# Kernel optimization log

Measured on AMD Instinct MI355X. Metric: run time of the kernel, lower is better.

Reference implementation:

```python
import jax, jax.numpy as jnp
import numpy as np

KINEMATIC_CHAIN = [[0, 2, 5, 8, 11], [0, 1, 4, 7, 10], [0, 3, 6, 9, 12, 15],
                   [9, 14, 17, 19, 21], [9, 13, 16, 18, 20]]
PATHS = [c[1:] for c in KINEMATIC_CHAIN]  # nb_joints == 22 branch


def _gauss_integral(s1, e1, s2, e2):
    # s1,e1,s2,e2: (..., 3) broadcastable; returns (...,) GLI per segment pair
    r13 = s2 - s1
    r14 = e2 - s1
    r23 = s2 - e1
    r24 = e2 - e1
    r12 = e1 - s1
    r34 = e2 - s2
    faces = jnp.stack([jnp.cross(r13, r14), jnp.cross(r14, r24),
                       jnp.cross(r24, r23), jnp.cross(r23, r13)], axis=-2)  # (...,4,3)
    norms = jnp.linalg.norm(faces, axis=-1, keepdims=True)
    nf = jnp.where(norms > 0, faces / jnp.maximum(norms, 1e-30), 0.0)
    dots = jnp.sum(nf * jnp.roll(nf, -1, axis=-2), axis=-1)  # (...,4)
    dots = jnp.clip(dots, -1.0 + 1e-7, 1.0 - 1e-7)
    gli = jnp.sum(jnp.arcsin(dots), axis=-1)
    sign = jnp.sum(jnp.cross(r34, r12) * r13, axis=-1)
    gli = gli * jnp.where(sign <= 0, -1.0, 1.0)
    return gli / (4.0 * jnp.pi)


def _gli_motion(motion1, motion2):
    # motion: (B, F, J, 3) -> (B, F, P*P) summed GLI per path pair
    pair_sums = []
    for p1 in PATHS:
        p1 = np.asarray(p1)
        s1 = motion1[:, :, p1[:-1], None, :]   # (B,F,n1,1,3)
        e1 = motion1[:, :, p1[1:], None, :]
        for p2 in PATHS:
            p2 = np.asarray(p2)
            s2 = motion2[:, :, None, p2[:-1], :]  # (B,F,1,n2,3)
            e2 = motion2[:, :, None, p2[1:], :]
            g = _gauss_integral(s1, e1, s2, e2)   # (B,F,n1,n2)
            pair_sums.append(jnp.sum(g, axis=(-1, -2)))
    return jnp.stack(pair_sums, axis=-1)  # (B, F, 25)


def setup_inputs() -> dict:
    key = jax.random.key(0)
    k1, k2 = jax.random.split(key)
    B, F, J = 32, 1024, 22
    return {
        "motion1": jax.random.normal(k1, (B, F, J, 3), dtype=jnp.float32),
        "motion2": jax.random.normal(k2, (B, F, J, 3), dtype=jnp.float32),
    }


def reference(motion1, motion2):
    gli = _gli_motion(motion1, motion2)            # (B, F, 25)
    vel = jnp.abs(gli[:, 1:] - gli[:, :-1])        # (B, F-1, 25)
    return jnp.max(vel, axis=-1)                   # (B, F-1)
```

## Files before the change

### kernel.cpp

```cpp
#include <hip/hip_runtime.h>
#include <hip/hip_bf16.h>


#define NF 1024
#define NB 32
#define FPB 16

__constant__ int c_seg_a[16] = {2,5,8,  1,4,7,  3,6,9,12,  14,17,19,  13,16,18};
__constant__ int c_seg_b[16] = {5,8,11, 4,7,10, 6,9,12,15, 17,19,21,  16,18,20};
__constant__ int c_seg_p[16] = {0,0,0,  1,1,1,  2,2,2,2,   3,3,3,     4,4,4};
__constant__ int c_grp_s[5]  = {0, 3, 6, 10, 13};
__constant__ int c_grp_e[5]  = {3, 6, 10, 13, 16};

struct V3 { float x, y, z; };

__device__ __forceinline__ V3 vsub(V3 a, V3 b) { return {a.x-b.x, a.y-b.y, a.z-b.z}; }
__device__ __forceinline__ V3 vcross(V3 a, V3 b) {
    return {fmaf(a.y, b.z, -a.z*b.y), fmaf(a.z, b.x, -a.x*b.z), fmaf(a.x, b.y, -a.y*b.x)};
}
__device__ __forceinline__ float vdot(V3 a, V3 b) {
    return fmaf(a.x, b.x, fmaf(a.y, b.y, a.z*b.z));
}

__device__ __forceinline__ float fast_asin(float x) {
    float ax = fabsf(x);
    float p = fmaf(ax, -0.0012624911f, 0.0066700901f);
    p = fmaf(ax, p, -0.0170881256f);
    p = fmaf(ax, p,  0.0308918810f);
    p = fmaf(ax, p, -0.0501743046f);
    p = fmaf(ax, p,  0.0889789874f);
    p = fmaf(ax, p, -0.2145988016f);
    p = fmaf(ax, p,  1.5707963050f);
    float r = fmaf(-__builtin_amdgcn_sqrtf(1.0f - ax), p, 1.57079632679f);
    return copysignf(r, x);
}

__global__ __launch_bounds__(256)
void gli_kernel(const float* __restrict__ m1, const float* __restrict__ m2,
                float* __restrict__ gli)
{
    __shared__ float smem[FPB * 66 * 2];
    float* j1 = smem;
    float* j2 = smem + FPB * 66;

    const int f0 = blockIdx.x * FPB;
    const int b  = blockIdx.y;
    const int t  = threadIdx.x;

    const size_t mbase = ((size_t)b * NF + f0) * 66;
    for (int i = t; i < FPB * 66; i += 256) {
        j1[i] = m1[mbase + i];
        j2[i] = m2[mbase + i];
    }
    __syncthreads();

    const int k  = t >> 4;
    const int i1 = t & 15;
    const float* J1 = j1 + k * 66;
    const float* J2 = j2 + k * 66;

    const int a1 = c_seg_a[i1] * 3, b1 = c_seg_b[i1] * 3;
    V3 S1{J1[a1], J1[a1+1], J1[a1+2]};
    V3 E1{J1[b1], J1[b1+1], J1[b1+2]};
    V3 r12 = vsub(E1, S1);

    float acc[5] = {0.0f, 0.0f, 0.0f, 0.0f, 0.0f};

#pragma unroll
    for (int i2 = 0; i2 < 16; ++i2) {
        const int a2 = c_seg_a[i2] * 3, b2 = c_seg_b[i2] * 3;
        V3 S2{J2[a2], J2[a2+1], J2[a2+2]};
        V3 E2{J2[b2], J2[b2+1], J2[b2+2]};

        V3 r13 = vsub(S2, S1);
        V3 r14 = vsub(E2, S1);
        V3 r23 = vsub(S2, E1);
        V3 r24 = vsub(E2, E1);
        V3 r34 = vsub(E2, S2);

        V3 c0 = vcross(r13, r14);
        V3 c1 = vcross(r14, r24);
        V3 c2 = vcross(r24, r23);
        V3 c3 = vcross(r23, r13);

        float n0 = vdot(c0, c0), n1 = vdot(c1, c1);
        float n2 = vdot(c2, c2), n3 = vdot(c3, c3);

        float q01 = n0 * n1, q12 = n1 * n2, q23 = n2 * n3, q30 = n3 * n0;
        float i01 = (q01 > 0.0f) ? __builtin_amdgcn_rsqf(q01) : 0.0f;
        float i12 = (q12 > 0.0f) ? __builtin_amdgcn_rsqf(q12) : 0.0f;
        float i23 = (q23 > 0.0f) ? __builtin_amdgcn_rsqf(q23) : 0.0f;
        float i30 = (q30 > 0.0f) ? __builtin_amdgcn_rsqf(q30) : 0.0f;

        const float lo = -1.0f + 1e-7f, hi = 1.0f - 1e-7f;
        float d0 = fminf(fmaxf(vdot(c0, c1) * i01, lo), hi);
        float d1 = fminf(fmaxf(vdot(c1, c2) * i12, lo), hi);
        float d2 = fminf(fmaxf(vdot(c2, c3) * i23, lo), hi);
        float d3 = fminf(fmaxf(vdot(c3, c0) * i30, lo), hi);

        float g = fast_asin(d0) + fast_asin(d1) + fast_asin(d2) + fast_asin(d3);

        float sgn = vdot(vcross(r34, r12), r13);
        g = (sgn <= 0.0f) ? -g : g;

        acc[c_seg_p[i2]] += g;
    }

    __syncthreads();

    float* red = smem;
#pragma unroll
    for (int p = 0; p < 5; ++p)
        red[(k * 16 + i1) * 5 + p] = acc[p] * 0.07957747154594767f;
    __syncthreads();

    for (int item = t; item < FPB * 25; item += 256) {
        int kk  = item / 25;
        int bin = item - kk * 25;
        int p1 = bin / 5, p2 = bin - p1 * 5;
        float s = 0.0f;
        for (int i = c_grp_s[p1]; i < c_grp_e[p1]; ++i)
            s += red[(kk * 16 + i) * 5 + p2];
        gli[((size_t)b * NF + f0 + kk) * 25 + bin] = s;
    }
}

__global__ __launch_bounds__(256)
void vel_kernel(const float* __restrict__ gli, float* __restrict__ out)
{
    const int f = blockIdx.x * blockDim.x + threadIdx.x;
    const int b = blockIdx.y;
    if (f >= NF - 1) return;

    const float* p0 = gli + ((size_t)b * NF + f) * 25;
    float m = 0.0f;
#pragma unroll
    for (int p = 0; p < 25; ++p)
        m = fmaxf(m, fabsf(p0[p + 25] - p0[p]));
    out[(size_t)b * (NF - 1) + f] = m;
}

extern "C" void kernel_launch(void* const* d_in, const int* in_sizes, int n_in,
                              void* d_out, int out_size, void* d_ws, size_t ws_size,
                              hipStream_t stream)
{
    const float* m1 = (const float*)d_in[0];
    const float* m2 = (const float*)d_in[1];
    float* out = (float*)d_out;
    float* gli = (float*)d_ws;

    hipLaunchKernelGGL(gli_kernel, dim3(NF / FPB, NB), dim3(256), 0, stream,
                       m1, m2, gli);
    hipLaunchKernelGGL(vel_kernel, dim3((NF - 1 + 255) / 256, NB), dim3(256),
                       0, stream, gli, out);
}
```

Before: 100.1 us.

## Pack two frames per thread with packed float2 math and transposed LDS layout

Each thread now handles the same segment pair for two adjacent frames, using 2-wide float vectors so the compiler can emit packed FMA/mul instructions on the cross/dot/asin polynomial work. Shared memory is transposed to joint-major with a padded stride so the two frames load as one 64-bit LDS read, and the block covers 32 frames instead of 16. This aims to halve VALU instruction count for the arithmetic-heavy inner loop, at the cost of more registers per thread and half as many blocks.

```diff
diff --git a/kernel.cpp b/kernel.cpp
--- a/kernel.cpp
+++ b/kernel.cpp
@@ -4,44 +4,62 @@
 
 #define NF 1024
 #define NB 32
-#define FPB 16
+#define FPB 32
 
-__constant__ int c_seg_a[16] = {2,5,8,  1,4,7,  3,6,9,12,  14,17,19,  13,16,18};
-__constant__ int c_seg_b[16] = {5,8,11, 4,7,10, 6,9,12,15, 17,19,21,  16,18,20};
-__constant__ int c_seg_p[16] = {0,0,0,  1,1,1,  2,2,2,2,   3,3,3,     4,4,4};
-__constant__ int c_grp_s[5]  = {0, 3, 6, 10, 13};
-__constant__ int c_grp_e[5]  = {3, 6, 10, 13, 16};
+typedef float v2f __attribute__((ext_vector_type(2)));
 
-struct V3 { float x, y, z; };
+struct W3 { v2f x, y, z; };
 
-__device__ __forceinline__ V3 vsub(V3 a, V3 b) { return {a.x-b.x, a.y-b.y, a.z-b.z}; }
-__device__ __forceinline__ V3 vcross(V3 a, V3 b) {
-    return {fmaf(a.y, b.z, -a.z*b.y), fmaf(a.z, b.x, -a.x*b.z), fmaf(a.x, b.y, -a.y*b.x)};
+__device__ __forceinline__ v2f FMA2(v2f a, v2f b, v2f c) {
+    return __builtin_elementwise_fma(a, b, c);
 }
-__device__ __forceinline__ float vdot(V3 a, V3 b) {
-    return fmaf(a.x, b.x, fmaf(a.y, b.y, a.z*b.z));
+__device__ __forceinline__ W3 wsub(W3 a, W3 b) { return {a.x-b.x, a.y-b.y, a.z-b.z}; }
+__device__ __forceinline__ W3 wcross(W3 a, W3 b) {
+    return { FMA2(a.y, b.z, -(a.z*b.y)),
+             FMA2(a.z, b.x, -(a.x*b.z)),
+             FMA2(a.x, b.y, -(a.y*b.x)) };
+}
+__device__ __forceinline__ v2f wdot(W3 a, W3 b) {
+    return FMA2(a.x, b.x, FMA2(a.y, b.y, a.z*b.z));
+}
+__device__ __forceinline__ v2f rsq_guard(v2f q) {
+    v2f r;
+    r.x = (q.x > 0.0f) ? __builtin_amdgcn_rsqf(q.x) : 0.0f;
+    r.y = (q.y > 0.0f) ? __builtin_amdgcn_rsqf(q.y) : 0.0f;
+    return r;
+}
+__device__ __forceinline__ v2f clamp2(v2f v) {
+    const float lo = -1.0f + 1e-7f, hi = 1.0f - 1e-7f;
+    v.x = fminf(fmaxf(v.x, lo), hi);
+    v.y = fminf(fmaxf(v.y, lo), hi);
+    return v;
+}
+__device__ __forceinline__ v2f asin2(v2f x) {
+    v2f ax; ax.x = fabsf(x.x); ax.y = fabsf(x.y);
+    v2f p = FMA2(ax, (v2f)(-0.0012624911f), (v2f)(0.0066700901f));
+    p = FMA2(ax, p, (v2f)(-0.0170881256f));
+    p = FMA2(ax, p, (v2f)( 0.0308918810f));
+    p = FMA2(ax, p, (v2f)(-0.0501743046f));
+    p = FMA2(ax, p, (v2f)( 0.0889789874f));
+    p = FMA2(ax, p, (v2f)(-0.2145988016f));
+    p = FMA2(ax, p, (v2f)( 1.5707963050f));
+    v2f om = (v2f)(1.0f) - ax;
+    v2f s; s.x = __builtin_amdgcn_sqrtf(om.x); s.y = __builtin_amdgcn_sqrtf(om.y);
+    v2f r = FMA2(-s, p, (v2f)(1.57079632679f));
+    r.x = copysignf(r.x, x.x);
+    r.y = copysignf(r.y, x.y);
+    return r;
 }
 
-__device__ __forceinline__ float fast_asin(float x) {
-    float ax = fabsf(x);
-    float p = fmaf(ax, -0.0012624911f, 0.0066700901f);
-    p = fmaf(ax, p, -0.0170881256f);
-    p = fmaf(ax, p,  0.0308918810f);
-    p = fmaf(ax, p, -0.0501743046f);
-    p = fmaf(ax, p,  0.0889789874f);
-    p = fmaf(ax, p, -0.2145988016f);
-    p = fmaf(ax, p,  1.5707963050f);
-    float r = fmaf(-__builtin_amdgcn_sqrtf(1.0f - ax), p, 1.57079632679f);
-    return copysignf(r, x);
-}
+#define JSTRIDE 34
 
 __global__ __launch_bounds__(256)
 void gli_kernel(const float* __restrict__ m1, const float* __restrict__ m2,
                 float* __restrict__ gli)
 {
-    __shared__ float smem[FPB * 66 * 2];
-    float* j1 = smem;
-    float* j2 = smem + FPB * 66;
+    __shared__ float smem[66 * JSTRIDE * 2];
+    float* jT1 = smem;
+    float* jT2 = smem + 66 * JSTRIDE;
 
     const int f0 = blockIdx.x * FPB;
     const int b  = blockIdx.y;
@@ -49,79 +67,90 @@
 
     const size_t mbase = ((size_t)b * NF + f0) * 66;
     for (int i = t; i < FPB * 66; i += 256) {
-        j1[i] = m1[mbase + i];
-        j2[i] = m2[mbase + i];
+        int f   = i / 66;
+        int off = i - f * 66;
+        jT1[off * JSTRIDE + f] = m1[mbase + i];
+        jT2[off * JSTRIDE + f] = m2[mbase + i];
     }
     __syncthreads();
 
-    const int k  = t >> 4;
+    constexpr int seg_a[16] = {2,5,8,  1,4,7,  3,6,9,12,  14,17,19,  13,16,18};
+    constexpr int seg_b[16] = {5,8,11, 4,7,10, 6,9,12,15, 17,19,21,  16,18,20};
+    constexpr int seg_p[16] = {0,0,0,  1,1,1,  2,2,2,2,   3,3,3,     4,4,4};
+
+    const int kp = t >> 4;
     const int i1 = t & 15;
-    const float* J1 = j1 + k * 66;
-    const float* J2 = j2 + k * 66;
+    const int fc = 2 * kp;
 
-    const int a1 = c_seg_a[i1] * 3, b1 = c_seg_b[i1] * 3;
-    V3 S1{J1[a1], J1[a1+1], J1[a1+2]};
-    V3 E1{J1[b1], J1[b1+1], J1[b1+2]};
-    V3 r12 = vsub(E1, S1);
+    const int a1 = seg_a[i1] * 3, b1 = seg_b[i1] * 3;
 
-    float acc[5] = {0.0f, 0.0f, 0.0f, 0.0f, 0.0f};
+    #define LD2(base, off) (*(const v2f*)&(base)[(off) * JSTRIDE + fc])
+    W3 S1{LD2(jT1, a1), LD2(jT1, a1+1), LD2(jT1, a1+2)};
+    W3 E1{LD2(jT1, b1), LD2(jT1, b1+1), LD2(jT1, b1+2)};
+    W3 r12 = wsub(E1, S1);
+
+    v2f acc[5] = {(v2f)(0.0f), (v2f)(0.0f), (v2f)(0.0f), (v2f)(0.0f), (v2f)(0.0f)};
 
 #pragma unroll
     for (int i2 = 0; i2 < 16; ++i2) {
-        const int a2 = c_seg_a[i2] * 3, b2 = c_seg_b[i2] * 3;
-        V3 S2{J2[a2], J2[a2+1], J2[a2+2]};
-        V3 E2{J2[b2], J2[b2+1], J2[b2+2]};
+        const int a2 = seg_a[i2] * 3, b2 = seg_b[i2] * 3;
+        W3 S2{LD2(jT2, a2), LD2(jT2, a2+1), LD2(jT2, a2+2)};
+        W3 E2{LD2(jT2, b2), LD2(jT2, b2+1), LD2(jT2, b2+2)};
 
-        V3 r13 = vsub(S2, S1);
-        V3 r14 = vsub(E2, S1);
-        V3 r23 = vsub(S2, E1);
-        V3 r24 = vsub(E2, E1);
-        V3 r34 = vsub(E2, S2);
+        W3 r13 = wsub(S2, S1);
+        W3 r14 = wsub(E2, S1);
+        W3 r23 = wsub(S2, E1);
+        W3 r24 = wsub(E2, E1);
+        W3 r34 = wsub(E2, S2);
 
-        V3 c0 = vcross(r13, r14);
-        V3 c1 = vcross(r14, r24);
-        V3 c2 = vcross(r24, r23);
-        V3 c3 = vcross(r23, r13);
+        W3 c0 = wcross(r13, r14);
+        W3 c1 = wcross(r14, r24);
+        W3 c2 = wcross(r24, r23);
+        W3 c3 = wcross(r23, r13);
 
-        float n0 = vdot(c0, c0), n1 = vdot(c1, c1);
-        float n2 = vdot(c2, c2), n3 = vdot(c3, c3);
+        v2f n0 = wdot(c0, c0), n1 = wdot(c1, c1);
+        v2f n2 = wdot(c2, c2), n3 = wdot(c3, c3);
 
-        float q01 = n0 * n1, q12 = n1 * n2, q23 = n2 * n3, q30 = n3 * n0;
-        float i01 = (q01 > 0.0f) ? __builtin_amdgcn_rsqf(q01) : 0.0f;
-        float i12 = (q12 > 0.0f) ? __builtin_amdgcn_rsqf(q12) : 0.0f;
-        float i23 = (q23 > 0.0f) ? __builtin_amdgcn_rsqf(q23) : 0.0f;
-        float i30 = (q30 > 0.0f) ? __builtin_amdgcn_rsqf(q30) : 0.0f;
+        v2f i01 = rsq_guard(n0 * n1);
+        v2f i12 = rsq_guard(n1 * n2);
+        v2f i23 = rsq_guard(n2 * n3);
+        v2f i30 = rsq_guard(n3 * n0);
 
-        const float lo = -1.0f + 1e-7f, hi = 1.0f - 1e-7f;
-        float d0 = fminf(fmaxf(vdot(c0, c1) * i01, lo), hi);
-        float d1 = fminf(fmaxf(vdot(c1, c2) * i12, lo), hi);
-        float d2 = fminf(fmaxf(vdot(c2, c3) * i23, lo), hi);
-        float d3 = fminf(fmaxf(vdot(c3, c0) * i30, lo), hi);
+        v2f d0 = clamp2(wdot(c0, c1) * i01);
+        v2f d1 = clamp2(wdot(c1, c2) * i12);
+        v2f d2 = clamp2(wdot(c2, c3) * i23);
+        v2f d3 = clamp2(wdot(c3, c0) * i30);
 
-        float g = fast_asin(d0) + fast_asin(d1) + fast_asin(d2) + fast_asin(d3);
+        v2f g = asin2(d0) + asin2(d1) + asin2(d2) + asin2(d3);
 
-        float sgn = vdot(vcross(r34, r12), r13);
-        g = (sgn <= 0.0f) ? -g : g;
+        v2f sgn = wdot(wcross(r34, r12), r13);
+        g.x = (sgn.x <= 0.0f) ? -g.x : g.x;
+        g.y = (sgn.y <= 0.0f) ? -g.y : g.y;
 
-        acc[c_seg_p[i2]] += g;
+        acc[seg_p[i2]] += g;
     }
+    #undef LD2
 
     __syncthreads();
 
     float* red = smem;
 #pragma unroll
-    for (int p = 0; p < 5; ++p)
-        red[(k * 16 + i1) * 5 + p] = acc[p] * 0.07957747154594767f;
+    for (int p = 0; p < 5; ++p) {
+        red[(fc    ) * 81 + i1 * 5 + p] = acc[p].x * 0.07957747154594767f;
+        red[(fc + 1) * 81 + i1 * 5 + p] = acc[p].y * 0.07957747154594767f;
+    }
     __syncthreads();
 
+    constexpr int grp_s[5] = {0, 3, 6, 10, 13};
+    constexpr int grp_e[5] = {3, 6, 10, 13, 16};
     for (int item = t; item < FPB * 25; item += 256) {
-        int kk  = item / 25;
-        int bin = item - kk * 25;
+        int f   = item / 25;
+        int bin = item - f * 25;
         int p1 = bin / 5, p2 = bin - p1 * 5;
         float s = 0.0f;
-        for (int i = c_grp_s[p1]; i < c_grp_e[p1]; ++i)
-            s += red[(kk * 16 + i) * 5 + p2];
-        gli[((size_t)b * NF + f0 + kk) * 25 + bin] = s;
+        for (int i = grp_s[p1]; i < grp_e[p1]; ++i)
+            s += red[f * 81 + i * 5 + p2];
+        gli[((size_t)b * NF + f0 + f) * 25 + bin] = s;
     }
 }
 
```

Measured after the change: 92.84 us. 7.3% less time.
